# Kernel optimization log

Hardware: AMD Instinct MI355X
Metric: run time of the kernel (lower is better)

## Reference

```python
import jax, jax.numpy as jnp
import numpy as np

NUM_NODES = 50000
NUM_EDGES = 800000
NUM_FEATURES = 128
HIDDEN = 256
NUM_CLASSES = 10
NUM_GRAPHS = 64


def setup_inputs() -> dict:
    key = jax.random.key(0)
    ks = jax.random.split(key, 16)
    x = jax.random.normal(ks[0], (NUM_NODES, NUM_FEATURES), dtype=jnp.float32)
    edge_index = jax.random.randint(ks[1], (2, NUM_EDGES), 0, NUM_NODES, dtype=jnp.int64)
    batch = jnp.sort(jax.random.randint(ks[2], (NUM_NODES,), 0, NUM_GRAPHS, dtype=jnp.int64))

    def glorot(k, shape):
        fan_in, fan_out = shape[-2], shape[-1]
        s = jnp.sqrt(6.0 / (fan_in + fan_out)).astype(jnp.float32)
        return jax.random.uniform(k, shape, jnp.float32, -s, s)

    inp = {
        "x": x, "edge_index": edge_index, "batch": batch,
        # Chebyshev weights: one [in, out] matrix per hop order k
        "W1": glorot(ks[3], (3, NUM_FEATURES, HIDDEN)), "b1": jnp.zeros((HIDDEN,), jnp.float32),
        "W2": glorot(ks[4], (4, HIDDEN, HIDDEN)),       "b2": jnp.zeros((HIDDEN,), jnp.float32),
        "W3": glorot(ks[5], (5, HIDDEN, HIDDEN)),       "b3": jnp.zeros((HIDDEN,), jnp.float32),
        "fc1_w": glorot(ks[6], (HIDDEN, 512)),  "fc1_b": jnp.zeros((512,), jnp.float32),
        "fc2_w": glorot(ks[7], (512, HIDDEN)),  "fc2_b": jnp.zeros((HIDDEN,), jnp.float32),
        "fc3_w": glorot(ks[8], (HIDDEN, NUM_CLASSES)), "fc3_b": jnp.zeros((NUM_CLASSES,), jnp.float32),
    }
    return inp


def reference(x, edge_index, batch, W1, b1, W2, b2, W3, b3,
              fc1_w, fc1_b, fc2_w, fc2_b, fc3_w, fc3_b):
    N = x.shape[0]
    src, dst = edge_index[0], edge_index[1]

    # Scaled Laplacian L_hat = -D^{-1/2} A D^{-1/2} (lambda_max = 2, sym norm)
    deg = jax.ops.segment_sum(jnp.ones_like(src, dtype=x.dtype), src, num_segments=N)
    dis = jnp.where(deg > 0, jax.lax.rsqrt(jnp.maximum(deg, 1.0)), 0.0)
    w = -dis[src] * dis[dst]  # [E]

    def prop(h):  # L_hat @ h via gather-scale-scatter
        return jax.ops.segment_sum(h[src] * w[:, None], dst, num_segments=N)

    def cheb(h, Wk, b):
        K = Wk.shape[0]
        Tx0 = h
        out = Tx0 @ Wk[0]
        Tx1 = prop(h)
        out = out + Tx1 @ Wk[1]
        for k in range(2, K):
            Tx2 = 2.0 * prop(Tx1) - Tx0
            out = out + Tx2 @ Wk[k]
            Tx0, Tx1 = Tx1, Tx2
        return out + b

    h = jax.nn.relu(cheb(x, W1, b1))
    h = jax.nn.relu(cheb(h, W2, b2))
    h = jax.nn.relu(cheb(h, W3, b3))

    # global mean pool over graphs in the batch
    sums = jax.ops.segment_sum(h, batch, num_segments=NUM_GRAPHS)
    cnts = jax.ops.segment_sum(jnp.ones((N,), h.dtype), batch, num_segments=NUM_GRAPHS)
    g = sums / jnp.maximum(cnts, 1.0)[:, None]  # [G, 256]

    g = jax.nn.relu(g @ fc1_w + fc1_b)  # dropout is identity at inference
    g = jax.nn.relu(g @ fc2_w + fc2_b)
    g = g @ fc3_w + fc3_b
    return jax.nn.log_softmax(g, axis=1)
```

## Files before the change

kernel.cpp:

```cpp
#include <hip/hip_runtime.h>
#include <cstdint>
#include <cstddef>

#define NN 50000
#define NE 800000
#define FIN 128
#define HID 256
#define NCLS 10
#define NG 64
#define LDT 1280

#define NCH 25
#define NCELL (NN * NCH)
#define NSCB ((NCELL + 255) / 256)

typedef unsigned int uint;
typedef unsigned short ushort;
typedef __attribute__((ext_vector_type(8))) short short8;
typedef __attribute__((ext_vector_type(4))) float f32x4;

static inline size_t align_up(size_t v, size_t a) { return (v + a - 1) / a * a; }

__device__ __forceinline__ float bf2f(ushort u) {
    union { uint i; float f; } v; v.i = (uint)u << 16; return v.f;
}
__device__ __forceinline__ ushort f2bf(float f) {
    union { uint i; float f; } v; v.f = f;
    uint i = v.i;
    uint r = (i + 0x7fffu + ((i >> 16) & 1u)) >> 16;
    return (ushort)r;
}
__device__ __forceinline__ uint pack2(float a, float b) {
    return (uint)f2bf(a) | ((uint)f2bf(b) << 16);
}


__global__ void k_degcnt(const int* __restrict__ src, const int* __restrict__ dst,
                         int* __restrict__ ideg, int* __restrict__ cellcnt) {
    int e = blockIdx.x * 256 + threadIdx.x;
    if (e < NE) {
        int s = src[e], d = dst[e];
        atomicAdd(&ideg[s], 1);
        atomicAdd(&cellcnt[d * NCH + (s >> 11)], 1);
    }
}

__global__ void k_dis(const int* __restrict__ ideg, float* __restrict__ dis) {
    int n = blockIdx.x * 256 + threadIdx.x;
    if (n < NN) {
        int d = ideg[n];
        dis[n] = (d > 0) ? rsqrtf((float)d) : 0.0f;
    }
}

__global__ void k_scanA(const int* __restrict__ cnt, int* __restrict__ rp,
                        int* __restrict__ bsum) {
    __shared__ int s[256];
    int i = blockIdx.x * 256 + threadIdx.x;
    int v = (i < NCELL) ? cnt[i] : 0;
    s[threadIdx.x] = v;
    __syncthreads();
    for (int off = 1; off < 256; off <<= 1) {
        int t = (threadIdx.x >= (unsigned)off) ? s[threadIdx.x - off] : 0;
        __syncthreads();
        s[threadIdx.x] += t;
        __syncthreads();
    }
    if (i < NCELL) rp[i] = s[threadIdx.x] - v;
    if (threadIdx.x == 255) bsum[blockIdx.x] = s[255];
}

__global__ void k_scanB(int* __restrict__ b, int n) {
    __shared__ int s[1024];
    __shared__ int carry;
    if (threadIdx.x == 0) carry = 0;
    __syncthreads();
    for (int base = 0; base < n; base += 1024) {
        int i = base + threadIdx.x;
        int v = (i < n) ? b[i] : 0;
        s[threadIdx.x] = v;
        __syncthreads();
        for (int off = 1; off < 1024; off <<= 1) {
            int t = (threadIdx.x >= (unsigned)off) ? s[threadIdx.x - off] : 0;
            __syncthreads();
            s[threadIdx.x] += t;
            __syncthreads();
        }
        int c = carry;
        if (i < n) b[i] = c + s[threadIdx.x] - v;
        __syncthreads();
        if (threadIdx.x == 0) carry = c + s[1023];
        __syncthreads();
    }
}

__global__ void k_scanC(const int* __restrict__ bsum, int* __restrict__ rp,
                        int* __restrict__ cur, int* __restrict__ rpn) {
    int i = blockIdx.x * 256 + threadIdx.x;
    if (i < NCELL) {
        int v = rp[i] + bsum[blockIdx.x];
        rp[i] = v;
        cur[i] = v;
        if (i % NCH == 0) rpn[i / NCH] = v;
    }
    if (i == 0) rpn[NN] = NE;
}

__global__ void k_fill2(const int* __restrict__ src, const int* __restrict__ dst,
                        const float* __restrict__ dis, int* __restrict__ cur,
                        uint2* __restrict__ em) {
    int e = blockIdx.x * 256 + threadIdx.x;
    if (e < NE) {
        int s = src[e], d = dst[e];
        int pos = atomicAdd(&cur[d * NCH + (s >> 11)], 1);
        uint2 m;
        m.x = (uint)s;
        m.y = __float_as_uint(-dis[s] * dis[d]);
        em[pos] = m;
    }
}

__global__ void k_wt(const float* __restrict__ W, ushort* __restrict__ Wt, int K) {
    int i = blockIdx.x * 256 + threadIdx.x;
    if (i < K * 256) {
        int k = i >> 8, n = i & 255;
        Wt[(size_t)n * K + k] = f2bf(W[i]);
    }
}


__global__ void k_spread_x(const float* __restrict__ x, ushort* __restrict__ T) {
    int i = blockIdx.x * 256 + threadIdx.x;
    if (i < NN * 64) {
        int m = i >> 6, p = i & 63;
        const float* xp = x + (size_t)m * FIN + p * 2;
        uint* tp = (uint*)(T + (size_t)m * LDT) + p;
        *tp = pack2(xp[0], xp[1]);
    }
}

__global__ void k_spread_h(const ushort* __restrict__ h, ushort* __restrict__ T) {
    int i = blockIdx.x * 256 + threadIdx.x;
    if (i < NN * 32) {
        int m = i >> 5, c = i & 31;
        const uint4* sp = (const uint4*)(h + (size_t)m * HID) + c;
        uint4* dp = (uint4*)(T + (size_t)m * LDT) + c;
        *dp = *sp;
    }
}

template <int FUSE, int F>
__global__ __launch_bounds__(512) void k_prop3(
    const int* __restrict__ rpn, const uint2* __restrict__ em,
    const ushort* __restrict__ h, const ushort* __restrict__ sub,
    ushort* __restrict__ out) {
    constexpr int NV = (F == 256) ? 4 : 2;
    int d = blockIdx.x * 8 + (threadIdx.x >> 6);
    int lane = threadIdx.x & 63;
    int beg = rpn[d], end = rpn[d + 1];
    float a[NV];
#pragma unroll
    for (int j = 0; j < NV; ++j) a[j] = 0.0f;

    int e = beg;
    for (; e + 4 <= end; e += 4) {
        uint2 m0 = em[e], m1 = em[e + 1], m2 = em[e + 2], m3 = em[e + 3];
        float w0 = __uint_as_float(m0.y), w1 = __uint_as_float(m1.y);
        float w2 = __uint_as_float(m2.y), w3 = __uint_as_float(m3.y);
        if (F == 256) {
            uint2 g0 = *((const uint2*)(h + (size_t)m0.x * LDT) + lane);
            uint2 g1 = *((const uint2*)(h + (size_t)m1.x * LDT) + lane);
            uint2 g2 = *((const uint2*)(h + (size_t)m2.x * LDT) + lane);
            uint2 g3 = *((const uint2*)(h + (size_t)m3.x * LDT) + lane);
            a[0] += w0 * bf2f((ushort)g0.x); a[1] += w0 * bf2f((ushort)(g0.x >> 16));
            a[2] += w0 * bf2f((ushort)g0.y); a[3] += w0 * bf2f((ushort)(g0.y >> 16));
            a[0] += w1 * bf2f((ushort)g1.x); a[1] += w1 * bf2f((ushort)(g1.x >> 16));
            a[2] += w1 * bf2f((ushort)g1.y); a[3] += w1 * bf2f((ushort)(g1.y >> 16));
            a[0] += w2 * bf2f((ushort)g2.x); a[1] += w2 * bf2f((ushort)(g2.x >> 16));
            a[2] += w2 * bf2f((ushort)g2.y); a[3] += w2 * bf2f((ushort)(g2.y >> 16));
            a[0] += w3 * bf2f((ushort)g3.x); a[1] += w3 * bf2f((ushort)(g3.x >> 16));
            a[2] += w3 * bf2f((ushort)g3.y); a[3] += w3 * bf2f((ushort)(g3.y >> 16));
        } else {
            uint g0 = *((const uint*)(h + (size_t)m0.x * LDT) + lane);
            uint g1 = *((const uint*)(h + (size_t)m1.x * LDT) + lane);
            uint g2 = *((const uint*)(h + (size_t)m2.x * LDT) + lane);
            uint g3 = *((const uint*)(h + (size_t)m3.x * LDT) + lane);
            a[0] += w0 * bf2f((ushort)g0); a[1] += w0 * bf2f((ushort)(g0 >> 16));
            a[0] += w1 * bf2f((ushort)g1); a[1] += w1 * bf2f((ushort)(g1 >> 16));
            a[0] += w2 * bf2f((ushort)g2); a[1] += w2 * bf2f((ushort)(g2 >> 16));
            a[0] += w3 * bf2f((ushort)g3); a[1] += w3 * bf2f((ushort)(g3 >> 16));
        }
    }
    for (; e < end; ++e) {
        uint2 m0 = em[e];
        float w0 = __uint_as_float(m0.y);
        if (F == 256) {
            uint2 g0 = *((const uint2*)(h + (size_t)m0.x * LDT) + lane);
            a[0] += w0 * bf2f((ushort)g0.x); a[1] += w0 * bf2f((ushort)(g0.x >> 16));
            a[2] += w0 * bf2f((ushort)g0.y); a[3] += w0 * bf2f((ushort)(g0.y >> 16));
        } else {
            uint g0 = *((const uint*)(h + (size_t)m0.x * LDT) + lane);
            a[0] += w0 * bf2f((ushort)g0); a[1] += w0 * bf2f((ushort)(g0 >> 16));
        }
    }

    if (F == 256) {
        uint2* op = (uint2*)(out + (size_t)d * LDT) + lane;
        if (FUSE) {
            uint2 sv = *((const uint2*)(sub + (size_t)d * LDT) + lane);
            uint2 r;
            r.x = pack2(2.0f * a[0] - bf2f((ushort)sv.x),
                        2.0f * a[1] - bf2f((ushort)(sv.x >> 16)));
            r.y = pack2(2.0f * a[2] - bf2f((ushort)sv.y),
                        2.0f * a[3] - bf2f((ushort)(sv.y >> 16)));
            *op = r;
        } else {
            uint2 r;
            r.x = pack2(a[0], a[1]);
            r.y = pack2(a[2], a[3]);
            *op = r;
        }
    } else {
        uint* op = (uint*)(out + (size_t)d * LDT) + lane;
        if (FUSE) {
            uint sv = *((const uint*)(sub + (size_t)d * LDT) + lane);
            *op = pack2(2.0f * a[0] - bf2f((ushort)sv),
                        2.0f * a[1] - bf2f((ushort)(sv >> 16)));
        } else {
            *op = pack2(a[0], a[1]);
        }
    }
}

__global__ __launch_bounds__(256) void k_mm_mfma(
    const ushort* __restrict__ A, int lda, int M, int K,
    const ushort* __restrict__ Wt, const float* __restrict__ bias,
    ushort* __restrict__ H) {
    __shared__ ushort As[128 * 32];
    __shared__ ushort Bs[128 * 32];
    int tid = threadIdx.x;
    int lane = tid & 63, w = tid >> 6;
    int wm = w >> 1, wn = w & 1;
    int rowBase = blockIdx.x * 128;
    int colBase = blockIdx.y * 128;
    f32x4 acc[4][4];
#pragma unroll
    for (int i = 0; i < 4; ++i)
#pragma unroll
        for (int j = 0; j < 4; ++j) acc[i][j] = (f32x4){0.f, 0.f, 0.f, 0.f};

    int srow = lane >> 2;
    int c16 = lane & 3;

    for (int k0 = 0; k0 < K; k0 += 32) {
#pragma unroll
        for (int q = 0; q < 2; ++q) {
            int seg = w * 2 + q;
            int r = seg * 16 + srow;
            int cs = c16 ^ ((r >> 1) & 3);
            int grow = rowBase + r;
            if (grow > M - 1) grow = M - 1;
            const ushort* gp = A + (size_t)grow * lda + k0 + cs * 8;
            __builtin_amdgcn_global_load_lds(
                (const __attribute__((address_space(1))) void*)gp,
                (__attribute__((address_space(3))) void*)((char*)As + seg * 1024),
                16, 0, 0);
        }
#pragma unroll
        for (int q = 0; q < 2; ++q) {
            int seg = w * 2 + q;
            int r = seg * 16 + srow;
            int cs = c16 ^ ((r >> 1) & 3);
            const ushort* gp = Wt + (size_t)(colBase + r) * K + k0 + cs * 8;
            __builtin_amdgcn_global_load_lds(
                (const __attribute__((address_space(1))) void*)gp,
                (__attribute__((address_space(3))) void*)((char*)Bs + seg * 1024),
                16, 0, 0);
        }
        __syncthreads();
        short8 af[4], bf[4];
#pragma unroll
        for (int mi = 0; mi < 4; ++mi) {
            int r = wm * 64 + mi * 16 + (lane & 15);
            int j = (lane >> 4) ^ ((r >> 1) & 3);
            af[mi] = *(const short8*)((const char*)As + r * 64 + j * 16);
        }
#pragma unroll
        for (int ni = 0; ni < 4; ++ni) {
            int r = wn * 64 + ni * 16 + (lane & 15);
            int j = (lane >> 4) ^ ((r >> 1) & 3);
            bf[ni] = *(const short8*)((const char*)Bs + r * 64 + j * 16);
        }
#pragma unroll
        for (int mi = 0; mi < 4; ++mi)
#pragma unroll
            for (int ni = 0; ni < 4; ++ni)
                acc[mi][ni] = __builtin_amdgcn_mfma_f32_16x16x32_bf16(
                    af[mi], bf[ni], acc[mi][ni], 0, 0, 0);
        __syncthreads();
    }
    int lg = lane >> 4;
    float bv[4];
#pragma unroll
    for (int ni = 0; ni < 4; ++ni)
        bv[ni] = bias[colBase + wn * 64 + ni * 16 + (lane & 15)];
#pragma unroll
    for (int mi = 0; mi < 4; ++mi) {
#pragma unroll
        for (int r = 0; r < 4; ++r) {
            int row = rowBase + wm * 64 + mi * 16 + lg * 4 + r;
            if (row >= M) continue;
#pragma unroll
            for (int ni = 0; ni < 4; ++ni) {
                int colL = colBase + wn * 64 + ni * 16 + (lane & 15);
                float v = acc[mi][ni][r] + bv[ni];
                v = fmaxf(v, 0.0f);
                H[(size_t)row * HID + colL] = f2bf(v);
            }
        }
    }
}


__global__ void k_pool(const ushort* __restrict__ h, const int* __restrict__ batch,
                       float* __restrict__ sums, float* __restrict__ cnts) {
    int f = threadIdx.x;
    int n0 = blockIdx.x * 128;
    if (n0 >= NN) return;
    int nEnd = n0 + 128 < NN ? n0 + 128 : NN;
    int cur = batch[n0];
    float acc = 0.0f, c = 0.0f;
    for (int n = n0; n < nEnd; ++n) {
        int b = batch[n];
        if (b != cur) {
            atomicAdd(&sums[cur * HID + f], acc);
            if (f == 0) atomicAdd(&cnts[cur], c);
            acc = 0.0f; c = 0.0f; cur = b;
        }
        acc += bf2f(h[(size_t)n * HID + f]);
        c += 1.0f;
    }
    atomicAdd(&sums[cur * HID + f], acc);
    if (f == 0) atomicAdd(&cnts[cur], c);
}

__global__ void k_gdiv(const float* __restrict__ sums, const float* __restrict__ cnts,
                       float* __restrict__ g) {
    int i = blockIdx.x * 256 + threadIdx.x;
    int b = i >> 8;
    g[i] = sums[i] / fmaxf(cnts[b], 1.0f);
}


template <int RELU>
__global__ void k_fc(const float* __restrict__ in, const float* __restrict__ W,
                     const float* __restrict__ bias, float* __restrict__ out,
                     int K, int Nc) {
    __shared__ float s[512];
    int gi = blockIdx.x;
    for (int i = threadIdx.x; i < K; i += blockDim.x) s[i] = in[gi * K + i];
    __syncthreads();
    int c = blockIdx.y * blockDim.x + threadIdx.x;
    if (c < Nc) {
        float acc = bias[c];
        for (int k = 0; k < K; ++k) acc += s[k] * W[k * Nc + c];
        out[gi * Nc + c] = RELU ? fmaxf(acc, 0.0f) : acc;
    }
}

__global__ void k_fc3_lsm(const float* __restrict__ in, const float* __restrict__ W,
                          const float* __restrict__ b, float* __restrict__ out) {
    __shared__ float s[HID];
    __shared__ float lg[NCLS];
    int gi = blockIdx.x;
    s[threadIdx.x] = in[gi * HID + threadIdx.x];
    __syncthreads();
    if (threadIdx.x < NCLS) {
        float acc = b[threadIdx.x];
        for (int k = 0; k < HID; ++k) acc += s[k] * W[k * NCLS + threadIdx.x];
        lg[threadIdx.x] = acc;
    }
    __syncthreads();
    if (threadIdx.x < NCLS) {
        float m = -1e30f;
        for (int c = 0; c < NCLS; ++c) m = fmaxf(m, lg[c]);
        float sum = 0.0f;
        for (int c = 0; c < NCLS; ++c) sum += expf(lg[c] - m);
        out[gi * NCLS + threadIdx.x] = lg[threadIdx.x] - m - logf(sum);
    }
}


extern "C" void kernel_launch(void* const* d_in, const int* in_sizes, int n_in,
                              void* d_out, int out_size, void* d_ws, size_t ws_size,
                              hipStream_t stream) {
    const float* x = (const float*)d_in[0];
    const int* ei = (const int*)d_in[1];
    const int* src = ei;
    const int* dst = ei + NE;
    const int* batch = (const int*)d_in[2];
    const float* W1 = (const float*)d_in[3];
    const float* b1 = (const float*)d_in[4];
    const float* W2 = (const float*)d_in[5];
    const float* b2 = (const float*)d_in[6];
    const float* W3 = (const float*)d_in[7];
    const float* b3 = (const float*)d_in[8];
    const float* fc1w = (const float*)d_in[9];
    const float* fc1b = (const float*)d_in[10];
    const float* fc2w = (const float*)d_in[11];
    const float* fc2b = (const float*)d_in[12];
    const float* fc3w = (const float*)d_in[13];
    const float* fc3b = (const float*)d_in[14];
    float* out = (float*)d_out;

    char* p = (char*)d_ws;
    auto carve = [&](size_t bytes) {
        char* r = p;
        p += align_up(bytes, 256);
        return (void*)r;
    };
    ushort* Tbig = (ushort*)carve((size_t)NN * LDT * 2);
    ushort* hA = (ushort*)carve((size_t)NN * HID * 2);
    ushort* hB = (ushort*)carve((size_t)NN * HID * 2);
    ushort* Wt1 = (ushort*)carve((size_t)HID * 384 * 2);
    ushort* Wt2 = (ushort*)carve((size_t)HID * 1024 * 2);
    ushort* Wt3 = (ushort*)carve((size_t)HID * 1280 * 2);
    int* ideg = (int*)carve((size_t)NN * 4);
    float* dis = (float*)carve((size_t)NN * 4);
    uint2* em = (uint2*)carve((size_t)NE * 8);
    int* cellcnt = (int*)carve((size_t)NCELL * 4);
    int* cellptr = (int*)carve((size_t)(NCELL + 1) * 4);
    int* ccur = (int*)carve((size_t)NCELL * 4);
    int* rpn = (int*)carve((size_t)(NN + 1) * 4);
    int* bsum = (int*)carve((size_t)NSCB * 4);
    float* psum = (float*)carve((size_t)NG * HID * 4);
    float* pcnt = (float*)carve((size_t)NG * 4);
    float* g = (float*)carve((size_t)NG * HID * 4);
    float* f1 = (float*)carve((size_t)NG * 512 * 4);
    float* f2 = (float*)carve((size_t)NG * HID * 4);

    hipMemsetAsync(ideg, 0, (size_t)NN * 4, stream);
    hipMemsetAsync(cellcnt, 0, (size_t)NCELL * 4, stream);
    hipMemsetAsync(psum, 0, (size_t)NG * HID * 4, stream);
    hipMemsetAsync(pcnt, 0, (size_t)NG * 4, stream);

    k_degcnt<<<(NE + 255) / 256, 256, 0, stream>>>(src, dst, ideg, cellcnt);
    k_dis<<<(NN + 255) / 256, 256, 0, stream>>>(ideg, dis);
    k_scanA<<<NSCB, 256, 0, stream>>>(cellcnt, cellptr, bsum);
    k_scanB<<<1, 1024, 0, stream>>>(bsum, NSCB);
    k_scanC<<<NSCB, 256, 0, stream>>>(bsum, cellptr, ccur, rpn);
    k_fill2<<<(NE + 255) / 256, 256, 0, stream>>>(src, dst, dis, ccur, em);

    k_wt<<<(384 * 256 + 255) / 256, 256, 0, stream>>>(W1, Wt1, 384);
    k_wt<<<(1024 * 256 + 255) / 256, 256, 0, stream>>>(W2, Wt2, 1024);
    k_wt<<<(1280 * 256 + 255) / 256, 256, 0, stream>>>(W3, Wt3, 1280);

    dim3 mmg((NN + 127) / 128, 2);

    k_spread_x<<<(NN * 64 + 255) / 256, 256, 0, stream>>>(x, Tbig);
    k_prop3<0, 128><<<NN / 8, 512, 0, stream>>>(rpn, em, Tbig + 0, nullptr, Tbig + 128);
    k_prop3<1, 128><<<NN / 8, 512, 0, stream>>>(rpn, em, Tbig + 128, Tbig + 0, Tbig + 256);
    k_mm_mfma<<<mmg, 256, 0, stream>>>(Tbig, LDT, NN, 384, Wt1, b1, hA);

    k_spread_h<<<(NN * 32 + 255) / 256, 256, 0, stream>>>(hA, Tbig);
    k_prop3<0, 256><<<NN / 8, 512, 0, stream>>>(rpn, em, Tbig + 0, nullptr, Tbig + 256);
    k_prop3<1, 256><<<NN / 8, 512, 0, stream>>>(rpn, em, Tbig + 256, Tbig + 0, Tbig + 512);
    k_prop3<1, 256><<<NN / 8, 512, 0, stream>>>(rpn, em, Tbig + 512, Tbig + 256, Tbig + 768);
    k_mm_mfma<<<mmg, 256, 0, stream>>>(Tbig, LDT, NN, 1024, Wt2, b2, hB);

    k_spread_h<<<(NN * 32 + 255) / 256, 256, 0, stream>>>(hB, Tbig);
    k_prop3<0, 256><<<NN / 8, 512, 0, stream>>>(rpn, em, Tbig + 0, nullptr, Tbig + 256);
    k_prop3<1, 256><<<NN / 8, 512, 0, stream>>>(rpn, em, Tbig + 256, Tbig + 0, Tbig + 512);
    k_prop3<1, 256><<<NN / 8, 512, 0, stream>>>(rpn, em, Tbig + 512, Tbig + 256, Tbig + 768);
    k_prop3<1, 256><<<NN / 8, 512, 0, stream>>>(rpn, em, Tbig + 768, Tbig + 512, Tbig + 1024);
    k_mm_mfma<<<mmg, 256, 0, stream>>>(Tbig, LDT, NN, 1280, Wt3, b3, hA);

    k_pool<<<(NN + 127) / 128, 256, 0, stream>>>(hA, batch, psum, pcnt);
    k_gdiv<<<(NG * HID) / 256, 256, 0, stream>>>(psum, pcnt, g);
    k_fc<1><<<dim3(NG, 2), 256, 0, stream>>>(g, fc1w, fc1b, f1, HID, 512);
    k_fc<1><<<dim3(NG, 1), 256, 0, stream>>>(f1, fc2w, fc2b, f2, 512, HID);
    k_fc3_lsm<<<NG, 256, 0, stream>>>(f2, fc3w, fc3b, out);
}
```

Baseline: 918.6 us.

## Write GEMM output into Chebyshev buffer slots, double-buffer GEMM, widen gather unroll

The GEMM kernel now takes per-slot column offsets, so each layer's output is written straight into a column slot of the big T buffer. This removes the spread copy kernels and the second hidden buffer, and the Chebyshev terms rotate through slots instead. The MFMA GEMM is templated on K and double-buffers its LDS tiles, overlapping the next tile's global-to-LDS load with compute. The propagation gather is unrolled by 8 to keep more loads in flight, and the source-chunk bucketing for edge sorting is coarsened from 25 to 13 chunks, which costs some gather locality in exchange for less scan and atomic work.

```diff
diff --git a/kernel.cpp b/kernel.cpp
--- a/kernel.cpp
+++ b/kernel.cpp
@@ -10,7 +10,7 @@
 #define NG 64
 #define LDT 1280
 
-#define NCH 25
+#define NCH 13
 #define NCELL (NN * NCH)
 #define NSCB ((NCELL + 255) / 256)
 
@@ -41,7 +41,7 @@
     if (e < NE) {
         int s = src[e], d = dst[e];
         atomicAdd(&ideg[s], 1);
-        atomicAdd(&cellcnt[d * NCH + (s >> 11)], 1);
+        atomicAdd(&cellcnt[d * NCH + (s >> 12)], 1);
     }
 }
 
@@ -112,7 +112,7 @@
     int e = blockIdx.x * 256 + threadIdx.x;
     if (e < NE) {
         int s = src[e], d = dst[e];
-        int pos = atomicAdd(&cur[d * NCH + (s >> 11)], 1);
+        int pos = atomicAdd(&cur[d * NCH + (s >> 12)], 1);
         uint2 m;
         m.x = (uint)s;
         m.y = __float_as_uint(-dis[s] * dis[d]);
@@ -136,16 +136,6 @@
         const float* xp = x + (size_t)m * FIN + p * 2;
         uint* tp = (uint*)(T + (size_t)m * LDT) + p;
         *tp = pack2(xp[0], xp[1]);
-    }
-}
-
-__global__ void k_spread_h(const ushort* __restrict__ h, ushort* __restrict__ T) {
-    int i = blockIdx.x * 256 + threadIdx.x;
-    if (i < NN * 32) {
-        int m = i >> 5, c = i & 31;
-        const uint4* sp = (const uint4*)(h + (size_t)m * HID) + c;
-        uint4* dp = (uint4*)(T + (size_t)m * LDT) + c;
-        *dp = *sp;
     }
 }
 
@@ -163,32 +153,64 @@
     for (int j = 0; j < NV; ++j) a[j] = 0.0f;
 
     int e = beg;
+    for (; e + 8 <= end; e += 8) {
+        uint2 mt[8];
+#pragma unroll
+        for (int u = 0; u < 8; ++u) mt[u] = em[e + u];
+        if (F == 256) {
+            uint2 gg[8];
+#pragma unroll
+            for (int u = 0; u < 8; ++u)
+                gg[u] = *((const uint2*)(h + (size_t)mt[u].x * LDT) + lane);
+#pragma unroll
+            for (int u = 0; u < 8; ++u) {
+                float wv = __uint_as_float(mt[u].y);
+                a[0] += wv * bf2f((ushort)gg[u].x);
+                a[1] += wv * bf2f((ushort)(gg[u].x >> 16));
+                a[2] += wv * bf2f((ushort)gg[u].y);
+                a[3] += wv * bf2f((ushort)(gg[u].y >> 16));
+            }
+        } else {
+            uint gg[8];
+#pragma unroll
+            for (int u = 0; u < 8; ++u)
+                gg[u] = *((const uint*)(h + (size_t)mt[u].x * LDT) + lane);
+#pragma unroll
+            for (int u = 0; u < 8; ++u) {
+                float wv = __uint_as_float(mt[u].y);
+                a[0] += wv * bf2f((ushort)gg[u]);
+                a[1] += wv * bf2f((ushort)(gg[u] >> 16));
+            }
+        }
+    }
     for (; e + 4 <= end; e += 4) {
-        uint2 m0 = em[e], m1 = em[e + 1], m2 = em[e + 2], m3 = em[e + 3];
-        float w0 = __uint_as_float(m0.y), w1 = __uint_as_float(m1.y);
-        float w2 = __uint_as_float(m2.y), w3 = __uint_as_float(m3.y);
+        uint2 mt[4];
+#pragma unroll
+        for (int u = 0; u < 4; ++u) mt[u] = em[e + u];
         if (F == 256) {
-            uint2 g0 = *((const uint2*)(h + (size_t)m0.x * LDT) + lane);
-            uint2 g1 = *((const uint2*)(h + (size_t)m1.x * LDT) + lane);
-            uint2 g2 = *((const uint2*)(h + (size_t)m2.x * LDT) + lane);
-            uint2 g3 = *((const uint2*)(h + (size_t)m3.x * LDT) + lane);
-            a[0] += w0 * bf2f((ushort)g0.x); a[1] += w0 * bf2f((ushort)(g0.x >> 16));
-            a[2] += w0 * bf2f((ushort)g0.y); a[3] += w0 * bf2f((ushort)(g0.y >> 16));
-            a[0] += w1 * bf2f((ushort)g1.x); a[1] += w1 * bf2f((ushort)(g1.x >> 16));
-            a[2] += w1 * bf2f((ushort)g1.y); a[3] += w1 * bf2f((ushort)(g1.y >> 16));
-            a[0] += w2 * bf2f((ushort)g2.x); a[1] += w2 * bf2f((ushort)(g2.x >> 16));
-            a[2] += w2 * bf2f((ushort)g2.y); a[3] += w2 * bf2f((ushort)(g2.y >> 16));
-            a[0] += w3 * bf2f((ushort)g3.x); a[1] += w3 * bf2f((ushort)(g3.x >> 16));
-            a[2] += w3 * bf2f((ushort)g3.y); a[3] += w3 * bf2f((ushort)(g3.y >> 16));
+            uint2 gg[4];
+#pragma unroll
+            for (int u = 0; u < 4; ++u)
+                gg[u] = *((const uint2*)(h + (size_t)mt[u].x * LDT) + lane);
+#pragma unroll
+            for (int u = 0; u < 4; ++u) {
+                float wv = __uint_as_float(mt[u].y);
+                a[0] += wv * bf2f((ushort)gg[u].x);
+                a[1] += wv * bf2f((ushort)(gg[u].x >> 16));
+                a[2] += wv * bf2f((ushort)gg[u].y);
+                a[3] += wv * bf2f((ushort)(gg[u].y >> 16));
+            }
         } else {
-            uint g0 = *((const uint*)(h + (size_t)m0.x * LDT) + lane);
-            uint g1 = *((const uint*)(h + (size_t)m1.x * LDT) + lane);
-            uint g2 = *((const uint*)(h + (size_t)m2.x * LDT) + lane);
-            uint g3 = *((const uint*)(h + (size_t)m3.x * LDT) + lane);
-            a[0] += w0 * bf2f((ushort)g0); a[1] += w0 * bf2f((ushort)(g0 >> 16));
-            a[0] += w1 * bf2f((ushort)g1); a[1] += w1 * bf2f((ushort)(g1 >> 16));
-            a[0] += w2 * bf2f((ushort)g2); a[1] += w2 * bf2f((ushort)(g2 >> 16));
-            a[0] += w3 * bf2f((ushort)g3); a[1] += w3 * bf2f((ushort)(g3 >> 16));
+            uint gg[4];
+#pragma unroll
+            for (int u = 0; u < 4; ++u)
+                gg[u] = *((const uint*)(h + (size_t)mt[u].x * LDT) + lane);
+#pragma unroll
+            for (int u = 0; u < 4; ++u) {
+                float wv = __uint_as_float(mt[u].y);
+                a[0] += wv * bf2f((ushort)gg[u]);
+                a[1] += wv * bf2f((ushort)(gg[u] >> 16));
+            }
         }
     }
     for (; e < end; ++e) {
@@ -232,27 +254,35 @@
     }
 }
 
-__global__ __launch_bounds__(256) void k_mm_mfma(
-    const ushort* __restrict__ A, int lda, int M, int K,
+template <int K>
+__global__ __launch_bounds__(256) void k_mm2(
+    const ushort* __restrict__ A, int lda,
+    int m0, int m1, int m2, int m3, int m4,
     const ushort* __restrict__ Wt, const float* __restrict__ bias,
-    ushort* __restrict__ H) {
-    __shared__ ushort As[128 * 32];
-    __shared__ ushort Bs[128 * 32];
+    ushort* __restrict__ H, int ldh, int M) {
+    constexpr int NT = K / 32;
+    __shared__ ushort As[2][128 * 32];
+    __shared__ ushort Bs[2][128 * 32];
     int tid = threadIdx.x;
     int lane = tid & 63, w = tid >> 6;
     int wm = w >> 1, wn = w & 1;
     int rowBase = blockIdx.x * 128;
     int colBase = blockIdx.y * 128;
-    f32x4 acc[4][4];
-#pragma unroll
-    for (int i = 0; i < 4; ++i)
-#pragma unroll
-        for (int j = 0; j < 4; ++j) acc[i][j] = (f32x4){0.f, 0.f, 0.f, 0.f};
-
     int srow = lane >> 2;
     int c16 = lane & 3;
 
-    for (int k0 = 0; k0 < K; k0 += 32) {
+    f32x4 acc[4][4];
+#pragma unroll
+    for (int i = 0; i < 4; ++i)
+#pragma unroll
+        for (int j = 0; j < 4; ++j) acc[i][j] = (f32x4){0.f, 0.f, 0.f, 0.f};
+
+    auto stage = [&](int t) {
+        int kk = t * 32;
+        int slot = kk >> 8;
+        int coff = (slot == 0 ? m0 : slot == 1 ? m1 : slot == 2 ? m2
+                    : slot == 3 ? m3 : m4) + (kk & 255);
+        int b = t & 1;
 #pragma unroll
         for (int q = 0; q < 2; ++q) {
             int seg = w * 2 + q;
@@ -260,10 +290,10 @@
             int cs = c16 ^ ((r >> 1) & 3);
             int grow = rowBase + r;
             if (grow > M - 1) grow = M - 1;
-            const ushort* gp = A + (size_t)grow * lda + k0 + cs * 8;
+            const ushort* gp = A + (size_t)grow * lda + coff + cs * 8;
             __builtin_amdgcn_global_load_lds(
                 (const __attribute__((address_space(1))) void*)gp,
-                (__attribute__((address_space(3))) void*)((char*)As + seg * 1024),
+                (__attribute__((address_space(3))) void*)((char*)&As[b][0] + seg * 1024),
                 16, 0, 0);
         }
 #pragma unroll
@@ -271,25 +301,33 @@
             int seg = w * 2 + q;
             int r = seg * 16 + srow;
             int cs = c16 ^ ((r >> 1) & 3);
-            const ushort* gp = Wt + (size_t)(colBase + r) * K + k0 + cs * 8;
+            const ushort* gp = Wt + (size_t)(colBase + r) * K + kk + cs * 8;
             __builtin_amdgcn_global_load_lds(
                 (const __attribute__((address_space(1))) void*)gp,
-                (__attribute__((address_space(3))) void*)((char*)Bs + seg * 1024),
+                (__attribute__((address_space(3))) void*)((char*)&Bs[b][0] + seg * 1024),
                 16, 0, 0);
         }
-        __syncthreads();
+    };
+
+    stage(0);
+    asm volatile("s_waitcnt vmcnt(0)" ::: "memory");
+    __builtin_amdgcn_s_barrier();
+
+    for (int t = 0; t < NT; ++t) {
+        if (t + 1 < NT) stage(t + 1);
+        int b = t & 1;
         short8 af[4], bf[4];
 #pragma unroll
         for (int mi = 0; mi < 4; ++mi) {
             int r = wm * 64 + mi * 16 + (lane & 15);
             int j = (lane >> 4) ^ ((r >> 1) & 3);
-            af[mi] = *(const short8*)((const char*)As + r * 64 + j * 16);
+            af[mi] = *(const short8*)((const char*)&As[b][0] + r * 64 + j * 16);
         }
 #pragma unroll
         for (int ni = 0; ni < 4; ++ni) {
             int r = wn * 64 + ni * 16 + (lane & 15);
             int j = (lane >> 4) ^ ((r >> 1) & 3);
-            bf[ni] = *(const short8*)((const char*)Bs + r * 64 + j * 16);
+            bf[ni] = *(const short8*)((const char*)&Bs[b][0] + r * 64 + j * 16);
         }
 #pragma unroll
         for (int mi = 0; mi < 4; ++mi)
@@ -297,8 +335,10 @@
             for (int ni = 0; ni < 4; ++ni)
                 acc[mi][ni] = __builtin_amdgcn_mfma_f32_16x16x32_bf16(
                     af[mi], bf[ni], acc[mi][ni], 0, 0, 0);
-        __syncthreads();
-    }
+        asm volatile("s_waitcnt vmcnt(0)" ::: "memory");
+        __builtin_amdgcn_s_barrier();
+    }
+
     int lg = lane >> 4;
     float bv[4];
 #pragma unroll
@@ -315,7 +355,7 @@
                 int colL = colBase + wn * 64 + ni * 16 + (lane & 15);
                 float v = acc[mi][ni][r] + bv[ni];
                 v = fmaxf(v, 0.0f);
-                H[(size_t)row * HID + colL] = f2bf(v);
+                H[(size_t)row * ldh + colL] = f2bf(v);
             }
         }
     }
@@ -421,7 +461,6 @@
     };
     ushort* Tbig = (ushort*)carve((size_t)NN * LDT * 2);
     ushort* hA = (ushort*)carve((size_t)NN * HID * 2);
-    ushort* hB = (ushort*)carve((size_t)NN * HID * 2);
     ushort* Wt1 = (ushort*)carve((size_t)HID * 384 * 2);
     ushort* Wt2 = (ushort*)carve((size_t)HID * 1024 * 2);
     ushort* Wt3 = (ushort*)carve((size_t)HID * 1280 * 2);
@@ -460,20 +499,21 @@
     k_spread_x<<<(NN * 64 + 255) / 256, 256, 0, stream>>>(x, Tbig);
     k_prop3<0, 128><<<NN / 8, 512, 0, stream>>>(rpn, em, Tbig + 0, nullptr, Tbig + 128);
     k_prop3<1, 128><<<NN / 8, 512, 0, stream>>>(rpn, em, Tbig + 128, Tbig + 0, Tbig + 256);
-    k_mm_mfma<<<mmg, 256, 0, stream>>>(Tbig, LDT, NN, 384, Wt1, b1, hA);
-
-    k_spread_h<<<(NN * 32 + 255) / 256, 256, 0, stream>>>(hA, Tbig);
-    k_prop3<0, 256><<<NN / 8, 512, 0, stream>>>(rpn, em, Tbig + 0, nullptr, Tbig + 256);
+    k_mm2<384><<<mmg, 256, 0, stream>>>(Tbig, LDT, 0, 256, 0, 0, 0,
+                                        Wt1, b1, Tbig + 1024, LDT, NN);
+
+    k_prop3<0, 256><<<NN / 8, 512, 0, stream>>>(rpn, em, Tbig + 1024, nullptr, Tbig + 0);
+    k_prop3<1, 256><<<NN / 8, 512, 0, stream>>>(rpn, em, Tbig + 0, Tbig + 1024, Tbig + 256);
     k_prop3<1, 256><<<NN / 8, 512, 0, stream>>>(rpn, em, Tbig + 256, Tbig + 0, Tbig + 512);
-    k_prop3<1, 256><<<NN / 8, 512, 0, stream>>>(rpn, em, Tbig + 512, Tbig + 256, Tbig + 768);
-    k_mm_mfma<<<mmg, 256, 0, stream>>>(Tbig, LDT, NN, 1024, Wt2, b2, hB);
-
-    k_spread_h<<<(NN * 32 + 255) / 256, 256, 0, stream>>>(hB, Tbig);
-    k_prop3<0, 256><<<NN / 8, 512, 0, stream>>>(rpn, em, Tbig + 0, nullptr, Tbig + 256);
+    k_mm2<1024><<<mmg, 256, 0, stream>>>(Tbig, LDT, 1024, 0, 256, 512, 0,
+                                         Wt2, b2, Tbig + 768, LDT, NN);
+
+    k_prop3<0, 256><<<NN / 8, 512, 0, stream>>>(rpn, em, Tbig + 768, nullptr, Tbig + 1024);
+    k_prop3<1, 256><<<NN / 8, 512, 0, stream>>>(rpn, em, Tbig + 1024, Tbig + 768, Tbig + 0);
+    k_prop3<1, 256><<<NN / 8, 512, 0, stream>>>(rpn, em, Tbig + 0, Tbig + 1024, Tbig + 256);
     k_prop3<1, 256><<<NN / 8, 512, 0, stream>>>(rpn, em, Tbig + 256, Tbig + 0, Tbig + 512);
-    k_prop3<1, 256><<<NN / 8, 512, 0, stream>>>(rpn, em, Tbig + 512, Tbig + 256, Tbig + 768);
-    k_prop3<1, 256><<<NN / 8, 512, 0, stream>>>(rpn, em, Tbig + 768, Tbig + 512, Tbig + 1024);
-    k_mm_mfma<<<mmg, 256, 0, stream>>>(Tbig, LDT, NN, 1280, Wt3, b3, hA);
+    k_mm2<1280><<<mmg, 256, 0, stream>>>(Tbig, LDT, 768, 1024, 0, 256, 512,
+                                         Wt3, b3, hA, HID, NN);
 
     k_pool<<<(NN + 127) / 128, 256, 0, stream>>>(hA, batch, psum, pcnt);
     k_gdiv<<<(NG * HID) / 256, 256, 0, stream>>>(psum, pcnt, g);
```

Measured after the change: 880.9 us. -4.1%, faster.
